# Optimization experiments

Hardware: AMD Instinct MI355X
Metric: run time of the kernel (lower is better)

Reference implementation:

```python
import jax, jax.numpy as jnp
import numpy as np

NUM_FEATURES = 20480
NUM_ACC = 128
BATCH = 4096
SPARSITY_P = 0.0015  # ~30 active features per position, like real NNUE


def setup_inputs() -> dict:
    key = jax.random.key(0)
    kw, kb, k1, k2, k3, k4 = jax.random.split(key, 6)
    # sparse binary one-hot-per-piece feature vectors
    white = (jax.random.uniform(kw, (BATCH, NUM_FEATURES)) < SPARSITY_P).astype(jnp.float32)
    black = (jax.random.uniform(kb, (BATCH, NUM_FEATURES)) < SPARSITY_P).astype(jnp.float32)
    psqt_w = jax.random.normal(k1, (2, NUM_FEATURES), dtype=jnp.float32) * 0.02
    acc_w = jax.random.normal(k2, (NUM_ACC, NUM_FEATURES), dtype=jnp.float32) * 0.02
    acc_b = jax.random.normal(k3, (NUM_ACC,), dtype=jnp.float32) * 0.02
    out_w = jax.random.normal(k4, (2, NUM_ACC), dtype=jnp.float32) * 0.1
    return {"white": white, "black": black, "psqt_w": psqt_w,
            "acc_w": acc_w, "acc_b": acc_b, "out_w": out_w}


def _side(x, psqt_w, acc_w, acc_b, out_w):
    # psqt: [B,2]; accumulator: [B,128]; CReLU then Linear(128->2, no bias)
    psqt = x @ psqt_w.T                              # [B, 2]
    acc = jnp.clip(x @ acc_w.T + acc_b, 0.0, 1.0)    # [B, 128]
    pos = acc @ out_w.T                              # [B, 2]
    return psqt, pos


def reference(white, black, psqt_w, acc_w, acc_b, out_w):
    psqt_w_, pos_w = _side(white, psqt_w, acc_w, acc_b, out_w)
    psqt_b, pos_b = _side(black, psqt_w, acc_w, acc_b, out_w)
    return (psqt_w_ - psqt_b) + (pos_w - pos_b)      # [B, 2]
```

## Files before the change

### kernel.cpp

```cpp
#include <hip/hip_runtime.h>

#define NF     20480
#define NACC   128
#define BATCH  4096
#define MAXI   96

typedef unsigned int uvec4 __attribute__((ext_vector_type(4)));

__device__ __forceinline__ float bflo(unsigned int w) {
    union { unsigned int u; float f; } v; v.u = w << 16; return v.f;
}
__device__ __forceinline__ float bfhi(unsigned int w) {
    union { unsigned int u; float f; } v; v.u = w & 0xFFFF0000u; return v.f;
}
__device__ __forceinline__ unsigned short f2bf(float f) {
    union { float f; unsigned int i; } v; v.f = f;
    unsigned int x = v.i;
    return (unsigned short)((x + 0x7FFFu + ((x >> 16) & 1u)) >> 16);
}

__global__ __launch_bounds__(256) void transpose_accw(const float* __restrict__ acc_w,
                                                      unsigned short* __restrict__ accT,
                                                      int* __restrict__ cnt) {
    if (blockIdx.x < 32) cnt[blockIdx.x * 256 + threadIdx.x] = 0;

    __shared__ float tile[NACC][33];
    const int t  = threadIdx.x;
    const int f0 = blockIdx.x * 32;
    const int fl = t & 31;
    const int cr = t >> 5;
    #pragma unroll
    for (int i = 0; i < 16; ++i) {
        int cc = i * 8 + cr;
        tile[cc][fl] = acc_w[(size_t)cc * NF + f0 + fl];
    }
    __syncthreads();
    const int c2 = t & 63;
    const int fr = t >> 6;
    #pragma unroll
    for (int i = 0; i < 8; ++i) {
        int ff = i * 4 + fr;
        unsigned int u = ((unsigned int)f2bf(tile[c2 * 2 + 1][ff]) << 16)
                       |  (unsigned int)f2bf(tile[c2 * 2][ff]);
        *(unsigned int*)(accT + (size_t)(f0 + ff) * NACC + c2 * 2) = u;
    }
}

#define EMIT(d, f)                                                        \
    if ((d) != 0u) {                                                      \
        int p = atomicAdd(mycnt, 1);                                      \
        if (p < MAXI) myidx[p] = (f);                                     \
    }

#define PROCQ(c, f0)                                                      \
    if (((c).x | (c).y | (c).z | (c).w) != 0u) {                          \
        EMIT((c).x, (f0) + 0)                                             \
        EMIT((c).y, (f0) + 1)                                             \
        EMIT((c).z, (f0) + 2)                                             \
        EMIT((c).w, (f0) + 3)                                             \
    }

__global__ __launch_bounds__(256) void nnue_scan(
    const float* __restrict__ white,
    const float* __restrict__ black,
    int* __restrict__ cnt,
    int* __restrict__ gidx)
{
    const int t    = threadIdx.x;
    const int b    = blockIdx.x;
    const int side = t >> 7;
    const int lt   = t & 127;

    const float* X  = (side ? black : white) + (size_t)b * NF;
    const uvec4* Xv = (const uvec4*)X;

    int* mycnt = cnt + side * BATCH + b;
    int* myidx = gidx + ((size_t)side * BATCH + b) * MAXI;

    uvec4 c0 = Xv[lt];
    uvec4 c1 = Xv[lt + 128];
    uvec4 c2 = Xv[lt + 256];
    uvec4 c3 = Xv[lt + 384];

    #pragma unroll 1
    for (int i = 0; i < 10; ++i) {
        uvec4 n0 = {0,0,0,0}, n1 = {0,0,0,0}, n2 = {0,0,0,0}, n3 = {0,0,0,0};
        if (i < 9) {
            const int v = (i + 1) * 512 + lt;
            n0 = Xv[v];
            n1 = Xv[v + 128];
            n2 = Xv[v + 256];
            n3 = Xv[v + 384];
        }
        const int fb = (i * 512 + lt) * 4;
        PROCQ(c0, fb)
        PROCQ(c1, fb + 512)
        PROCQ(c2, fb + 1024)
        PROCQ(c3, fb + 1536)
        c0 = n0; c1 = n1; c2 = n2; c3 = n3;
    }
}

__global__ __launch_bounds__(256) void nnue_out(
    const float* __restrict__ psqt_w,
    const unsigned short* __restrict__ accT,
    const float* __restrict__ acc_b,
    const float* __restrict__ out_w,
    const int* __restrict__ cnt,
    const int* __restrict__ gidx,
    float* __restrict__ out)
{
    __shared__ int   s_list[2][MAXI];
    __shared__ float s_part[2][2][NACC];
    __shared__ float s_red[8];

    const int t    = threadIdx.x;
    const int b    = blockIdx.x;
    const int side = t >> 7;
    const int wv   = (t >> 6) & 1;
    const int lt   = t & 127;
    const int lane = t & 63;

    const int n = min(cnt[side * BATCH + b], MAXI);
    const int* myidx = gidx + ((size_t)side * BATCH + b) * MAXI;
    if (lt < n) s_list[side][lt] = myidx[lt];
    __syncthreads();

    float ps0 = 0.f, ps1 = 0.f;
    if (lt < n) {
        int f = s_list[side][lt];
        ps0 = psqt_w[f];
        ps1 = psqt_w[NF + f];
    }

    float a0 = 0.f, a1 = 0.f;
    #pragma unroll 2
    for (int j = wv; j < n; j += 2) {
        int f = s_list[side][j];
        unsigned int w = *(const unsigned int*)(accT + (size_t)f * NACC + lane * 2);
        a0 += bflo(w); a1 += bfhi(w);
    }
    s_part[side][wv][lane * 2]     = a0;
    s_part[side][wv][lane * 2 + 1] = a1;
    __syncthreads();

    const float bias = acc_b[lt];
    const float ow0  = out_w[lt];
    const float ow1  = out_w[NACC + lt];
    const float sgn  = side ? -1.f : 1.f;

    float a  = s_part[side][0][lt] + s_part[side][1][lt];
    float h  = fminf(fmaxf(a + bias, 0.f), 1.f);
    float p0 = sgn * (h * ow0 + ps0);
    float p1 = sgn * (h * ow1 + ps1);

    #pragma unroll
    for (int off = 32; off > 0; off >>= 1) {
        p0 += __shfl_down(p0, off, 64);
        p1 += __shfl_down(p1, off, 64);
    }
    if ((t & 63) == 0) { int w8 = t >> 6; s_red[w8 * 2] = p0; s_red[w8 * 2 + 1] = p1; }
    __syncthreads();

    if (t == 0) {
        out[(size_t)b * 2 + 0] = s_red[0] + s_red[2] + s_red[4] + s_red[6];
        out[(size_t)b * 2 + 1] = s_red[1] + s_red[3] + s_red[5] + s_red[7];
    }
}

extern "C" void kernel_launch(void* const* d_in, const int* in_sizes, int n_in,
                              void* d_out, int out_size, void* d_ws, size_t ws_size,
                              hipStream_t stream) {
    const float* white  = (const float*)d_in[0];
    const float* black  = (const float*)d_in[1];
    const float* psqt_w = (const float*)d_in[2];
    const float* acc_w  = (const float*)d_in[3];
    const float* acc_b  = (const float*)d_in[4];
    const float* out_w  = (const float*)d_in[5];
    float* out = (float*)d_out;

    unsigned short* accT = (unsigned short*)d_ws;
    int* cnt  = (int*)((char*)d_ws + 5242880);
    int* gidx = (int*)((char*)d_ws + 5242880 + 32768);

    transpose_accw<<<NF / 32, 256, 0, stream>>>(acc_w, accT, cnt);
    nnue_scan<<<BATCH, 256, 0, stream>>>(white, black, cnt, gidx);
    nnue_out<<<BATCH, 256, 0, stream>>>(psqt_w, accT, acc_b, out_w,
                                        cnt, gidx, out);
}
```

Baseline: 662.0 us.

## Flatten sparse scan into grid-strided streaming with nontemporal loads

The scan kernel no longer assigns one block per batch row. It runs a fixed 2048x256 grid that walks white and then black as flat arrays with grid-stride nontemporal vector loads, and it works out the batch row and feature index by division for each nonzero chunk. The goal is fully coalesced streaming of the two large dense inputs with fewer blocks and no cache pollution. The gather loop unroll also goes from 2 to 4. The atomic index order within a row becomes less deterministic, which is harmless because the later summation does not depend on order.

```diff
diff --git a/kernel.cpp b/kernel.cpp
--- a/kernel.cpp
+++ b/kernel.cpp
@@ -1,9 +1,13 @@
 #include <hip/hip_runtime.h>
 
 #define NF     20480
+#define NFV4   5120
 #define NACC   128
 #define BATCH  4096
 #define MAXI   96
+#define SCANB  2048
+#define SCANT  256
+#define STRIDE (SCANB * SCANT)
 
 typedef unsigned int uvec4 __attribute__((ext_vector_type(4)));
 
@@ -48,17 +52,47 @@
 
 #define EMIT(d, f)                                                        \
     if ((d) != 0u) {                                                      \
-        int p = atomicAdd(mycnt, 1);                                      \
-        if (p < MAXI) myidx[p] = (f);                                     \
+        int p = atomicAdd(cn, 1);                                         \
+        if (p < MAXI) ix[p] = (f);                                        \
     }
 
-#define PROCQ(c, f0)                                                      \
-    if (((c).x | (c).y | (c).z | (c).w) != 0u) {                          \
-        EMIT((c).x, (f0) + 0)                                             \
-        EMIT((c).y, (f0) + 1)                                             \
-        EMIT((c).z, (f0) + 2)                                             \
-        EMIT((c).w, (f0) + 3)                                             \
+#define PROCQ(c, gexpr)                                                   \
+    {                                                                     \
+        if (((c).x | (c).y | (c).z | (c).w) != 0u) {                      \
+            const int g  = (gexpr);                                       \
+            const int b  = g / NFV4;                                      \
+            const int f0 = (g - b * NFV4) * 4;                            \
+            int* cn = cnt + side * BATCH + b;                             \
+            int* ix = gidx + (side * BATCH + b) * MAXI;                   \
+            EMIT((c).x, f0)     EMIT((c).y, f0 + 1)                       \
+            EMIT((c).z, f0 + 2) EMIT((c).w, f0 + 3)                       \
+        }                                                                 \
     }
+
+__device__ __forceinline__ void scan_flat(const uvec4* __restrict__ Xv, int tid, int side,
+                                          int* __restrict__ cnt, int* __restrict__ gidx) {
+    uvec4 c0 = __builtin_nontemporal_load(&Xv[tid]);
+    uvec4 c1 = __builtin_nontemporal_load(&Xv[tid + STRIDE]);
+    uvec4 c2 = __builtin_nontemporal_load(&Xv[tid + 2 * STRIDE]);
+    uvec4 c3 = __builtin_nontemporal_load(&Xv[tid + 3 * STRIDE]);
+
+    #pragma unroll 1
+    for (int i = 0; i < 10; ++i) {
+        uvec4 n0 = {0,0,0,0}, n1 = {0,0,0,0}, n2 = {0,0,0,0}, n3 = {0,0,0,0};
+        if (i < 9) {
+            const int j = tid + (4 * i + 4) * STRIDE;
+            n0 = __builtin_nontemporal_load(&Xv[j]);
+            n1 = __builtin_nontemporal_load(&Xv[j + STRIDE]);
+            n2 = __builtin_nontemporal_load(&Xv[j + 2 * STRIDE]);
+            n3 = __builtin_nontemporal_load(&Xv[j + 3 * STRIDE]);
+        }
+        PROCQ(c0, tid + (4 * i + 0) * STRIDE)
+        PROCQ(c1, tid + (4 * i + 1) * STRIDE)
+        PROCQ(c2, tid + (4 * i + 2) * STRIDE)
+        PROCQ(c3, tid + (4 * i + 3) * STRIDE)
+        c0 = n0; c1 = n1; c2 = n2; c3 = n3;
+    }
+}
 
 __global__ __launch_bounds__(256) void nnue_scan(
     const float* __restrict__ white,
@@ -66,39 +100,9 @@
     int* __restrict__ cnt,
     int* __restrict__ gidx)
 {
-    const int t    = threadIdx.x;
-    const int b    = blockIdx.x;
-    const int side = t >> 7;
-    const int lt   = t & 127;
-
-    const float* X  = (side ? black : white) + (size_t)b * NF;
-    const uvec4* Xv = (const uvec4*)X;
-
-    int* mycnt = cnt + side * BATCH + b;
-    int* myidx = gidx + ((size_t)side * BATCH + b) * MAXI;
-
-    uvec4 c0 = Xv[lt];
-    uvec4 c1 = Xv[lt + 128];
-    uvec4 c2 = Xv[lt + 256];
-    uvec4 c3 = Xv[lt + 384];
-
-    #pragma unroll 1
-    for (int i = 0; i < 10; ++i) {
-        uvec4 n0 = {0,0,0,0}, n1 = {0,0,0,0}, n2 = {0,0,0,0}, n3 = {0,0,0,0};
-        if (i < 9) {
-            const int v = (i + 1) * 512 + lt;
-            n0 = Xv[v];
-            n1 = Xv[v + 128];
-            n2 = Xv[v + 256];
-            n3 = Xv[v + 384];
-        }
-        const int fb = (i * 512 + lt) * 4;
-        PROCQ(c0, fb)
-        PROCQ(c1, fb + 512)
-        PROCQ(c2, fb + 1024)
-        PROCQ(c3, fb + 1536)
-        c0 = n0; c1 = n1; c2 = n2; c3 = n3;
-    }
+    const int tid = blockIdx.x * SCANT + threadIdx.x;
+    scan_flat((const uvec4*)white, tid, 0, cnt, gidx);
+    scan_flat((const uvec4*)black, tid, 1, cnt, gidx);
 }
 
 __global__ __launch_bounds__(256) void nnue_out(
@@ -134,7 +138,7 @@
     }
 
     float a0 = 0.f, a1 = 0.f;
-    #pragma unroll 2
+    #pragma unroll 4
     for (int j = wv; j < n; j += 2) {
         int f = s_list[side][j];
         unsigned int w = *(const unsigned int*)(accT + (size_t)f * NACC + lane * 2);
@@ -184,7 +188,7 @@
     int* gidx = (int*)((char*)d_ws + 5242880 + 32768);
 
     transpose_accw<<<NF / 32, 256, 0, stream>>>(acc_w, accT, cnt);
-    nnue_scan<<<BATCH, 256, 0, stream>>>(white, black, cnt, gidx);
+    nnue_scan<<<SCANB, SCANT, 0, stream>>>(white, black, cnt, gidx);
     nnue_out<<<BATCH, 256, 0, stream>>>(psqt_w, accT, acc_b, out_w,
                                         cnt, gidx, out);
 }
```

Result: faster. 638.7 us (-3.5%).
